# Performance work log

Measured on AMD Instinct MI355X. Metric: run time of the kernel, lower is better.

## Reference

```python
import jax, jax.numpy as jnp
import numpy as np

N_HEADS = 16

def setup_inputs() -> dict:
    key = jax.random.key(0)
    ks = jax.random.split(key, 5)
    D = 1024
    B, T = 4, 1024
    scale = 1.0 / np.sqrt(D)
    x = jax.random.normal(ks[0], (B, T, D), dtype=jnp.float32)
    Wq = jax.random.normal(ks[1], (D, D), dtype=jnp.float32) * scale
    Wk = jax.random.normal(ks[2], (D, D), dtype=jnp.float32) * scale
    Wv = jax.random.normal(ks[3], (D, D), dtype=jnp.float32) * scale
    Wo = jax.random.normal(ks[4], (D, D), dtype=jnp.float32) * scale
    return {"x": x, "Wq": Wq, "Wk": Wk, "Wv": Wv, "Wo": Wo}


def reference(x, Wq, Wk, Wv, Wo):
    # FLA BasedLinearAttention (mode='chunk', normalize=True, scale=1) with
    # Taylor feature map phi(u) = [1, u/d^{1/4}, (u (x) u)/sqrt(2 d)], so
    # phi(q)·phi(k) = 1 + s + s^2/2 where s = (q·k)/sqrt(d).
    B, T, D = x.shape
    H = N_HEADS
    d = D // H  # head_dim == feature_dim
    # torch Linear: y = x @ W.T (bias=False in FLA proj layers)
    q = (x @ Wq.T).reshape(B, T, H, d).transpose(0, 2, 1, 3)  # b h t d
    k = (x @ Wk.T).reshape(B, T, H, d).transpose(0, 2, 1, 3)
    v = (x @ Wv.T).reshape(B, T, H, d).transpose(0, 2, 1, 3)
    s = jnp.einsum('bhtd,bhsd->bhts', q, k) / jnp.sqrt(jnp.float32(d))
    scores = 1.0 + s + 0.5 * s * s  # always > 0 (= ((s+1)^2+1)/2)
    causal = jnp.tril(jnp.ones((T, T), dtype=bool))
    scores = jnp.where(causal, scores, 0.0)
    num = jnp.einsum('bhts,bhsd->bhtd', scores, v)
    den = jnp.sum(scores, axis=-1, keepdims=True)
    o = num / den  # b h t d
    o = o.transpose(0, 2, 1, 3).reshape(B, T, D)  # b t (h d)
    return o @ Wo.T
```

## Files before the change

### kernel.cpp

```cpp
#include <hip/hip_runtime.h>

typedef unsigned short u16;
typedef __attribute__((ext_vector_type(8))) short bf16x8;
typedef __attribute__((ext_vector_type(8))) unsigned short u16x8;
typedef __attribute__((ext_vector_type(4))) float f32x4;

#define MFMA16(a, b, c) __builtin_amdgcn_mfma_f32_16x16x32_bf16((a), (b), (c), 0, 0, 0)

__device__ __forceinline__ void gll16(const void* g, void* l) {
    __builtin_amdgcn_global_load_lds(
        (const __attribute__((address_space(1))) unsigned int*)g,
        (__attribute__((address_space(3))) unsigned int*)l, 16, 0, 0);
}

__device__ __forceinline__ u16 f2b(float f) {
    unsigned int u = __float_as_uint(f);
    u += 0x7fffu + ((u >> 16) & 1u);
    return (u16)(u >> 16);
}

__device__ __forceinline__ unsigned int pkbf(float a, float b) {
    return (unsigned int)f2b(a) | ((unsigned int)f2b(b) << 16);
}

__global__ __launch_bounds__(256) void cast_all(const float* __restrict__ x,
                                                const float* __restrict__ w0,
                                                const float* __restrict__ w1,
                                                const float* __restrict__ w2,
                                                const float* __restrict__ w3,
                                                u16* __restrict__ xb,
                                                u16* __restrict__ wb) {
    const int bid = blockIdx.x;
    const float* s; u16* d; int off;
    if (bid < 2048) { s = x; d = xb; off = bid; }
    else {
        const int wi = (bid - 2048) >> 9;
        s = (wi == 0) ? w0 : (wi == 1) ? w1 : (wi == 2) ? w2 : w3;
        d = wb + (size_t)wi * 1048576;
        off = (bid - 2048) & 511;
    }
    const int i = (off * 256 + threadIdx.x) * 8;
    float4 a = *(const float4*)(s + i);
    float4 b = *(const float4*)(s + i + 4);
    *(uint4*)(d + i) = make_uint4(pkbf(a.x, a.y), pkbf(a.z, a.w),
                                  pkbf(b.x, b.y), pkbf(b.z, b.w));
}

template <int BN, int MODE>
__global__ __launch_bounds__(256) void gemm_bt(const u16* __restrict__ A,
                                               const u16* __restrict__ W,
                                               void* __restrict__ Yv,
                                               u16* __restrict__ vT,
                                               int K, int ldY) {
    __shared__ u16 As[128 * 32];
    __shared__ u16 Bs[BN * 32];
    constexpr int MI = (BN == 128) ? 4 : 2;
    const int t = threadIdx.x, w = t >> 6, lane = t & 63;
    const int quad = lane >> 4, m16 = lane & 15;
    const int wr = (BN == 128) ? ((w >> 1) * 64) : (w * 32);
    const int wc = (BN == 128) ? ((w & 1) * 64) : 0;
    const int row0 = blockIdx.x * 128, col0 = blockIdx.y * BN;
    const int srow = lane >> 2;
    const int scol = (lane & 3) * 8;

    f32x4 acc[MI][4];
#pragma unroll
    for (int i = 0; i < MI; ++i)
#pragma unroll
        for (int j = 0; j < 4; ++j) acc[i][j] = (f32x4){0.f, 0.f, 0.f, 0.f};

    for (int k0 = 0; k0 < K; k0 += 32) {
        if constexpr (BN == 128) {
#pragma unroll
            for (int cc = 0; cc < 2; ++cc) {
                const int c = w * 2 + cc;
                const int rr = c * 16 + srow;
                gll16(A + (size_t)(row0 + rr) * K + k0 + scol, &As[c * 512]);
                gll16(W + (size_t)(col0 + rr) * K + k0 + scol, &Bs[c * 512]);
            }
        } else {
#pragma unroll
            for (int cc = 0; cc < 2; ++cc) {
                const int c = w * 2 + cc;
                const int rr = c * 16 + srow;
                gll16(A + (size_t)(row0 + rr) * K + k0 + scol, &As[c * 512]);
            }
            {
                const int rr = w * 16 + srow;
                gll16(W + (size_t)(col0 + rr) * K + k0 + scol, &Bs[w * 512]);
            }
        }
        __syncthreads();
        bf16x8 af[MI], bf[4];
#pragma unroll
        for (int i = 0; i < MI; ++i)
            af[i] = *(const bf16x8*)&As[(wr + i * 16 + m16) * 32 + quad * 8];
#pragma unroll
        for (int j = 0; j < 4; ++j)
            bf[j] = *(const bf16x8*)&Bs[(wc + j * 16 + m16) * 32 + quad * 8];
#pragma unroll
        for (int i = 0; i < MI; ++i)
#pragma unroll
            for (int j = 0; j < 4; ++j) acc[i][j] = MFMA16(af[i], bf[j], acc[i][j]);
        __syncthreads();
    }
    if constexpr (MODE == 0) {
#pragma unroll
        for (int i = 0; i < MI; ++i)
#pragma unroll
            for (int j = 0; j < 4; ++j)
#pragma unroll
                for (int r = 0; r < 4; ++r)
                    ((float*)Yv)[(size_t)(row0 + wr + i * 16 + quad * 4 + r) * ldY +
                                 col0 + wc + j * 16 + m16] = acc[i][j][r];
    } else {
        if (col0 < 2048) {
            u16* qk = (u16*)Yv;
#pragma unroll
            for (int i = 0; i < MI; ++i)
#pragma unroll
                for (int j = 0; j < 4; ++j)
#pragma unroll
                    for (int r = 0; r < 4; ++r)
                        qk[(size_t)(row0 + wr + i * 16 + quad * 4 + r) * 2048 +
                           col0 + wc + j * 16 + m16] = f2b(acc[i][j][r]);
        } else {
#pragma unroll
            for (int i = 0; i < MI; ++i) {
                const int rbase = row0 + wr + i * 16;
                const int bb = rbase >> 10;
                const int tok0 = (rbase & 1023) + quad * 4;
#pragma unroll
                for (int j = 0; j < 4; ++j) {
                    const int vTrow = bb * 1024 + (col0 + wc + j * 16 + m16 - 2048);
                    *(uint2*)(vT + (size_t)vTrow * 1024 + tok0) =
                        make_uint2(pkbf(acc[i][j][0], acc[i][j][1]),
                                   pkbf(acc[i][j][2], acc[i][j][3]));
                }
            }
        }
    }
}

__global__ __launch_bounds__(256) void based_attn(const u16* __restrict__ qkm,
                                                  const u16* __restrict__ vT,
                                                  u16* __restrict__ o) {
    __shared__ u16 qsA[2][64][32];
    __shared__ u16 qsB[2][64][32];
    __shared__ u16 ks[2][2][64][32];
    __shared__ u16 vs[2][2][64][32];
    __shared__ u16 Ss[2][64][32];

    const int t = threadIdx.x, w = t >> 6, lane = t & 63;
    const int quad = lane >> 4, m16 = lane & 15;
    const int p = blockIdx.x, h = blockIdx.y, b = blockIdx.z;
    const int tA = p, tB = 15 - p;
    const int srow = lane >> 2, s8 = (lane & 3) * 8;

    const size_t qbase = (size_t)b * 1024 * 2048 + h * 64;
    const size_t kbase = qbase + 1024;
    const size_t vbase = ((size_t)b * 1024 + h * 64) * 1024;

#pragma unroll
    for (int cc = 0; cc < 4; ++cc) {
        const int c = w * 4 + cc;
        const int tile = c >> 3, dblk = (c >> 2) & 1, rc = c & 3;
        const int Q0 = (tile ? tB : tA) * 64;
        gll16(qkm + qbase + (size_t)(Q0 + rc * 16 + srow) * 2048 + dblk * 32 + s8,
              tile ? &qsB[dblk][rc * 16][0] : &qsA[dblk][rc * 16][0]);
    }
#pragma unroll
    for (int cc = 0; cc < 2; ++cc) {
        const int c = w * 2 + cc;
        const int blk = c >> 2, rc = c & 3;
        gll16(qkm + kbase + (size_t)(rc * 16 + srow) * 2048 + blk * 32 + s8,
              &ks[0][blk][rc * 16][0]);
        gll16(vT + vbase + (size_t)(rc * 16 + srow) * 1024 + blk * 32 + s8,
              &vs[0][blk][rc * 16][0]);
    }

    bf16x8 ones;
#pragma unroll
    for (int e = 0; e < 8; ++e) ones[e] = (short)0x3F80;

    f32x4 numA[4], numB[4], denA, denB;
    denA = denB = (f32x4){0.f, 0.f, 0.f, 0.f};
#pragma unroll
    for (int j = 0; j < 4; ++j) numA[j] = numB[j] = (f32x4){0.f, 0.f, 0.f, 0.f};

#define TILE_COMPUTE(QS, NUM, DEN, DIAG)                                        \
    {                                                                           \
        f32x4 sacc[4];                                                          \
        _Pragma("unroll")                                                       \
        for (int jk = 0; jk < 4; ++jk) sacc[jk] = (f32x4){0.f, 0.f, 0.f, 0.f};  \
        _Pragma("unroll")                                                       \
        for (int kd = 0; kd < 2; ++kd) {                                        \
            bf16x8 qf = *(const bf16x8*)&QS[kd][w * 16 + m16][quad * 8];        \
            _Pragma("unroll")                                                   \
            for (int jk = 0; jk < 4; ++jk) {                                    \
                bf16x8 af = *(const bf16x8*)&ks[buf][kd][jk * 16 + m16][quad * 8]; \
                sacc[jk] = MFMA16(af, qf, sacc[jk]);                            \
            }                                                                   \
        }                                                                       \
        _Pragma("unroll")                                                       \
        for (int jk = 0; jk < 4; ++jk) {                                        \
            float sc[4];                                                        \
            _Pragma("unroll")                                                   \
            for (int r = 0; r < 4; ++r) {                                       \
                const float u = fmaf(sacc[jk][r], 0.125f, 1.0f);                \
                sc[r] = fmaf(u * 0.5f, u, 0.5f);                                \
            }                                                                   \
            if (DIAG) {                                                         \
                const int key0 = jk * 16 + quad * 4, qr = w * 16 + m16;         \
                _Pragma("unroll")                                               \
                for (int r = 0; r < 4; ++r)                                     \
                    if (key0 + r > qr) sc[r] = 0.f;                             \
            }                                                                   \
            const int kl = jk * 16 + quad * 4;                                  \
            *(uint2*)&Ss[kl >> 5][w * 16 + m16][kl & 31] =                      \
                make_uint2(pkbf(sc[0], sc[1]), pkbf(sc[2], sc[3]));             \
        }                                                                       \
        _Pragma("unroll")                                                       \
        for (int kb = 0; kb < 2; ++kb) {                                        \
            bf16x8 sf = *(const bf16x8*)&Ss[kb][w * 16 + m16][quad * 8];        \
            _Pragma("unroll")                                                   \
            for (int j = 0; j < 4; ++j) {                                       \
                bf16x8 vf = *(const bf16x8*)&vs[buf][kb][j * 16 + m16][quad * 8]; \
                NUM[j] = MFMA16(sf, vf, NUM[j]);                                \
            }                                                                   \
            DEN = MFMA16(sf, ones, DEN);                                        \
        }                                                                       \
    }

    for (int kt = 0; kt <= tB; ++kt) {
        const int buf = kt & 1;
        __syncthreads();
        if (kt < tB) {
            const int nb = buf ^ 1, kn = kt + 1;
#pragma unroll
            for (int cc = 0; cc < 2; ++cc) {
                const int c = w * 2 + cc;
                const int blk = c >> 2, rc = c & 3;
                gll16(qkm + kbase + (size_t)(kn * 64 + rc * 16 + srow) * 2048 + blk * 32 + s8,
                      &ks[nb][blk][rc * 16][0]);
                gll16(vT + vbase + (size_t)(rc * 16 + srow) * 1024 + kn * 64 + blk * 32 + s8,
                      &vs[nb][blk][rc * 16][0]);
            }
        }
        TILE_COMPUTE(qsB, numB, denB, (kt == tB));
        if (kt <= tA) TILE_COMPUTE(qsA, numA, denA, (kt == tA));
    }
#undef TILE_COMPUTE

#pragma unroll
    for (int r = 0; r < 4; ++r) {
        const float invA = 1.0f / denA[r], invB = 1.0f / denB[r];
        const int rowoff = w * 16 + quad * 4 + r;
        const size_t tokA = (size_t)(b * 1024 + tA * 64 + rowoff);
        const size_t tokB = (size_t)(b * 1024 + tB * 64 + rowoff);
#pragma unroll
        for (int j = 0; j < 4; ++j) {
            o[tokA * 1024 + h * 64 + j * 16 + m16] = f2b(numA[j][r] * invA);
            o[tokB * 1024 + h * 64 + j * 16 + m16] = f2b(numB[j][r] * invB);
        }
    }
}

extern "C" void kernel_launch(void* const* d_in, const int* in_sizes, int n_in,
                              void* d_out, int out_size, void* d_ws, size_t ws_size,
                              hipStream_t stream) {
    const float* x  = (const float*)d_in[0];
    const float* Wq = (const float*)d_in[1];
    const float* Wk = (const float*)d_in[2];
    const float* Wv = (const float*)d_in[3];
    const float* Wo = (const float*)d_in[4];
    float* out = (float*)d_out;

    const size_t MEL = 4096ull * 1024ull;
    u16* xb   = (u16*)d_ws;
    u16* Wqkv = xb + MEL;
    u16* Wob  = Wqkv + 3ull * 1024 * 1024;
    u16* qk   = Wob + 1024ull * 1024;
    u16* vT   = qk + 2ull * MEL;
    u16* o    = vT + MEL;

    cast_all<<<4096, 256, 0, stream>>>(x, Wq, Wk, Wv, Wo, xb, Wqkv);

    dim3 gq(32, 24);
    gemm_bt<128, 1><<<gq, 256, 0, stream>>>(xb, Wqkv, qk, vT, 1024, 2048);

    dim3 ga(8, 16, 4);
    based_attn<<<ga, 256, 0, stream>>>(qk, vT, o);

    dim3 go(32, 16);
    gemm_bt<64, 0><<<go, 256, 0, stream>>>(o, Wob, (void*)out, nullptr, 1024, 1024);
}
```

Measured before the change: 170.7 us.

## Double-buffer GEMM LDS tiles and use 64x64 tiles for output projection

The bf16 GEMM kernel now uses two LDS buffers and prefetches the next K-slice with global_load_lds while MFMAs run on the current one. This drops one of the two barriers per iteration. The output projection switches from 128x64 to 64x64 tiles on a doubled grid (1024 blocks), giving more parallelism. The cost is doubled LDS use and a smaller per-block tile for the second GEMM, which lowers data reuse.

```diff
diff --git a/kernel.cpp b/kernel.cpp
--- a/kernel.cpp
+++ b/kernel.cpp
@@ -46,69 +46,64 @@
                                   pkbf(b.x, b.y), pkbf(b.z, b.w));
 }
 
-template <int BN, int MODE>
+template <int BM, int BN, int MODE>
 __global__ __launch_bounds__(256) void gemm_bt(const u16* __restrict__ A,
                                                const u16* __restrict__ W,
                                                void* __restrict__ Yv,
                                                u16* __restrict__ vT,
                                                int K, int ldY) {
-    __shared__ u16 As[128 * 32];
-    __shared__ u16 Bs[BN * 32];
-    constexpr int MI = (BN == 128) ? 4 : 2;
+    constexpr int MI = BM / 32, NJ = BN / 32;
+    constexpr int ACH = BM / 16;
+    constexpr int NPW = (BM + BN) / 64;
+    __shared__ u16 As[2][BM * 32];
+    __shared__ u16 Bs[2][BN * 32];
     const int t = threadIdx.x, w = t >> 6, lane = t & 63;
     const int quad = lane >> 4, m16 = lane & 15;
-    const int wr = (BN == 128) ? ((w >> 1) * 64) : (w * 32);
-    const int wc = (BN == 128) ? ((w & 1) * 64) : 0;
-    const int row0 = blockIdx.x * 128, col0 = blockIdx.y * BN;
-    const int srow = lane >> 2;
-    const int scol = (lane & 3) * 8;
-
-    f32x4 acc[MI][4];
+    const int wr = (w >> 1) * (BM / 2), wc = (w & 1) * (BN / 2);
+    const int row0 = blockIdx.x * BM, col0 = blockIdx.y * BN;
+    const int srow = lane >> 2, scol = (lane & 3) * 8;
+
+    auto stage = [&](int buf, int k0) {
+#pragma unroll
+        for (int cc = 0; cc < NPW; ++cc) {
+            const int c = w * NPW + cc;
+            if (c < ACH)
+                gll16(A + (size_t)(row0 + c * 16 + srow) * K + k0 + scol,
+                      &As[buf][c * 512]);
+            else
+                gll16(W + (size_t)(col0 + (c - ACH) * 16 + srow) * K + k0 + scol,
+                      &Bs[buf][(c - ACH) * 512]);
+        }
+    };
+
+    f32x4 acc[MI][NJ];
 #pragma unroll
     for (int i = 0; i < MI; ++i)
 #pragma unroll
-        for (int j = 0; j < 4; ++j) acc[i][j] = (f32x4){0.f, 0.f, 0.f, 0.f};
-
+        for (int j = 0; j < NJ; ++j) acc[i][j] = (f32x4){0.f, 0.f, 0.f, 0.f};
+
+    stage(0, 0);
     for (int k0 = 0; k0 < K; k0 += 32) {
-        if constexpr (BN == 128) {
-#pragma unroll
-            for (int cc = 0; cc < 2; ++cc) {
-                const int c = w * 2 + cc;
-                const int rr = c * 16 + srow;
-                gll16(A + (size_t)(row0 + rr) * K + k0 + scol, &As[c * 512]);
-                gll16(W + (size_t)(col0 + rr) * K + k0 + scol, &Bs[c * 512]);
-            }
-        } else {
-#pragma unroll
-            for (int cc = 0; cc < 2; ++cc) {
-                const int c = w * 2 + cc;
-                const int rr = c * 16 + srow;
-                gll16(A + (size_t)(row0 + rr) * K + k0 + scol, &As[c * 512]);
-            }
-            {
-                const int rr = w * 16 + srow;
-                gll16(W + (size_t)(col0 + rr) * K + k0 + scol, &Bs[w * 512]);
-            }
-        }
+        const int buf = (k0 >> 5) & 1;
         __syncthreads();
-        bf16x8 af[MI], bf[4];
+        if (k0 + 32 < K) stage(buf ^ 1, k0 + 32);
+        bf16x8 af[MI], bf[NJ];
 #pragma unroll
         for (int i = 0; i < MI; ++i)
-            af[i] = *(const bf16x8*)&As[(wr + i * 16 + m16) * 32 + quad * 8];
-#pragma unroll
-        for (int j = 0; j < 4; ++j)
-            bf[j] = *(const bf16x8*)&Bs[(wc + j * 16 + m16) * 32 + quad * 8];
+            af[i] = *(const bf16x8*)&As[buf][(wr + i * 16 + m16) * 32 + quad * 8];
+#pragma unroll
+        for (int j = 0; j < NJ; ++j)
+            bf[j] = *(const bf16x8*)&Bs[buf][(wc + j * 16 + m16) * 32 + quad * 8];
 #pragma unroll
         for (int i = 0; i < MI; ++i)
 #pragma unroll
-            for (int j = 0; j < 4; ++j) acc[i][j] = MFMA16(af[i], bf[j], acc[i][j]);
-        __syncthreads();
+            for (int j = 0; j < NJ; ++j) acc[i][j] = MFMA16(af[i], bf[j], acc[i][j]);
     }
     if constexpr (MODE == 0) {
 #pragma unroll
         for (int i = 0; i < MI; ++i)
 #pragma unroll
-            for (int j = 0; j < 4; ++j)
+            for (int j = 0; j < NJ; ++j)
 #pragma unroll
                 for (int r = 0; r < 4; ++r)
                     ((float*)Yv)[(size_t)(row0 + wr + i * 16 + quad * 4 + r) * ldY +
@@ -119,7 +114,7 @@
 #pragma unroll
             for (int i = 0; i < MI; ++i)
 #pragma unroll
-                for (int j = 0; j < 4; ++j)
+                for (int j = 0; j < NJ; ++j)
 #pragma unroll
                     for (int r = 0; r < 4; ++r)
                         qk[(size_t)(row0 + wr + i * 16 + quad * 4 + r) * 2048 +
@@ -131,7 +126,7 @@
                 const int bb = rbase >> 10;
                 const int tok0 = (rbase & 1023) + quad * 4;
 #pragma unroll
-                for (int j = 0; j < 4; ++j) {
+                for (int j = 0; j < NJ; ++j) {
                     const int vTrow = bb * 1024 + (col0 + wc + j * 16 + m16 - 2048);
                     *(uint2*)(vT + (size_t)vTrow * 1024 + tok0) =
                         make_uint2(pkbf(acc[i][j][0], acc[i][j][1]),
@@ -287,11 +282,11 @@
     cast_all<<<4096, 256, 0, stream>>>(x, Wq, Wk, Wv, Wo, xb, Wqkv);
 
     dim3 gq(32, 24);
-    gemm_bt<128, 1><<<gq, 256, 0, stream>>>(xb, Wqkv, qk, vT, 1024, 2048);
+    gemm_bt<128, 128, 1><<<gq, 256, 0, stream>>>(xb, Wqkv, qk, vT, 1024, 2048);
 
     dim3 ga(8, 16, 4);
     based_attn<<<ga, 256, 0, stream>>>(qk, vT, o);
 
-    dim3 go(32, 16);
-    gemm_bt<64, 0><<<go, 256, 0, stream>>>(o, Wob, (void*)out, nullptr, 1024, 1024);
-}
+    dim3 go(64, 16);
+    gemm_bt<64, 64, 0><<<go, 256, 0, stream>>>(o, Wob, (void*)out, nullptr, 1024, 1024);
+}
```

Result: faster. 165.3 us (-3.1%).
